# Kernel tuning notes

Measured on AMD Instinct MI355X. Metric: run time of the kernel, lower is better.

The kernel has to match this reference:

```python
import jax, jax.numpy as jnp
import numpy as np


def setup_inputs() -> dict:
    key = jax.random.key(0)
    k1, k2, k3, k4, k5 = jax.random.split(key, 5)
    B, C, Q, E = 16, 2048, 128, 200
    x_contexts = jax.random.normal(k1, (B, C, E), dtype=jnp.float32)
    x_questions = jax.random.normal(k2, (B, Q, E), dtype=jnp.float32)
    # nn.Linear(3E, 1, bias=False) weight: (1, 3E)
    w_sim = jax.random.normal(k3, (1, 3 * E), dtype=jnp.float32) * (1.0 / np.sqrt(3 * E))
    # nn.Linear(4E, 128) weight: (128, 4E), bias: (128,)
    w_proj = jax.random.normal(k4, (128, 4 * E), dtype=jnp.float32) * (1.0 / np.sqrt(4 * E))
    b_proj = jax.random.normal(k5, (128,), dtype=jnp.float32) * 0.01
    return {"x_contexts": x_contexts, "x_questions": x_questions,
            "w_sim": w_sim, "w_proj": w_proj, "b_proj": b_proj}


def reference(x_contexts, x_questions, w_sim, w_proj, b_proj):
    E = x_contexts.shape[-1]
    # Decompose w_sim . [c; q; c*q] into three small contractions — same math,
    # avoids materializing the (B, C, Q, 3E) broadcast tensor of the original.
    w1, w2, w3 = w_sim[0, :E], w_sim[0, E:2 * E], w_sim[0, 2 * E:]
    s_c = jnp.einsum('bce,e->bc', x_contexts, w1)            # (B, C)
    s_q = jnp.einsum('bqe,e->bq', x_questions, w2)           # (B, Q)
    s_cq = jnp.einsum('bce,bqe->bcq', x_contexts * w3, x_questions)  # (B, C, Q)
    scores = s_cq + s_c[:, :, None] + s_q[:, None, :]        # (B, C, Q)

    S1 = jax.nn.softmax(scores, axis=-1)   # softmax over question words
    S2 = jax.nn.softmax(scores, axis=-2)   # softmax over context words

    c2q = jnp.einsum('bcq,bqe->bce', S1, x_questions)        # (B, C, E)
    # q2c = (S1 @ S2^T) @ contexts; contract small E last to keep (B,C,C) single pass
    S1S2T = jnp.einsum('bcq,bdq->bcd', S1, S2)               # (B, C, C)
    q2c = jnp.einsum('bcd,bde->bce', S1S2T, x_contexts)      # (B, C, E)

    feats = jnp.concatenate(
        [x_contexts, c2q, x_contexts * c2q, x_contexts * q2c], axis=-1)  # (B, C, 4E)
    return jnp.einsum('bcf,of->bco', feats, w_proj) + b_proj  # (B, C, 128)
```

## Files before the change

kernel.cpp:

```cpp
#include <hip/hip_runtime.h>
#include <hip/hip_bf16.h>

#define Bn 16
#define Cn 2048
#define Qn 128
#define En 200
#define Fn 800
#define On 128
#define EP 208

typedef float f32x4 __attribute__((ext_vector_type(4)));
typedef __bf16 bf16x8 __attribute__((ext_vector_type(8)));

__device__ __forceinline__ unsigned short f2bf(float f) {
    union { float f; unsigned u; } v; v.f = f;
    unsigned r = v.u + 0x7FFF + ((v.u >> 16) & 1);
    return (unsigned short)(r >> 16);
}
__device__ __forceinline__ float bf2f(unsigned short h) {
    union { unsigned u; float f; } v; v.u = (unsigned)h << 16;
    return v.f;
}
__device__ __forceinline__ bf16x8 mul8(bf16x8 a, bf16x8 b) {
    bf16x8 o;
#pragma unroll
    for (int k = 0; k < 8; ++k) o[k] = (__bf16)((float)a[k] * (float)b[k]);
    return o;
}
__device__ __forceinline__ bf16x8 scale8(bf16x8 a, float s) {
    bf16x8 o;
#pragma unroll
    for (int k = 0; k < 8; ++k) o[k] = (__bf16)((float)a[k] * s);
    return o;
}

__global__ __launch_bounds__(256) void k_prep_all(const float* __restrict__ xq,
                                                  const float* __restrict__ wsim,
                                                  const float* __restrict__ wp,
                                                  const float* __restrict__ xc,
                                                  unsigned short* __restrict__ yqb,
                                                  float* __restrict__ s_q,
                                                  unsigned short* __restrict__ wpb,
                                                  unsigned short* __restrict__ xqaT,
                                                  unsigned short* __restrict__ xcb,
                                                  unsigned short* __restrict__ xcT) {
    int bx = blockIdx.x;
    if (bx < 512) {
        int wid = (bx * 256 + threadIdx.x) >> 6;
        int lane = threadIdx.x & 63;
        const float* xrow = xq + (size_t)wid * En;
        float s = 0.f;
        for (int e = lane; e < En; e += 64) {
            float x = xrow[e];
            yqb[(size_t)wid * En + e] = f2bf(x * wsim[400 + e] + wsim[e]);
            s += x * wsim[200 + e];
        }
        for (int i = 32; i; i >>= 1) s += __shfl_xor(s, i, 64);
        if (lane == 0) s_q[wid] = s;
    } else if (bx < 612) {
        int gid = (bx - 512) * 256 + threadIdx.x;
        int base = gid * 4;
        if (base < On * Fn) {
            float4 v = *(const float4*)(wp + base);
            ushort4 o;
            o.x = f2bf(v.x); o.y = f2bf(v.y); o.z = f2bf(v.z); o.w = f2bf(v.w);
            *(ushort4*)(wpb + base) = o;
        }
    } else if (bx < 740) {
        int lb = bx - 612;
        int et = lb & 3, qt = (lb >> 2) & 1, b = lb >> 3;
        int e0 = et * 64, q0 = qt * 64;
        int tid = threadIdx.x;
        __shared__ float t[64][65];
        for (int i = tid; i < 64 * 64; i += 256) {
            int qi = i >> 6, ei = i & 63;
            int e = e0 + ei;
            t[qi][ei] = (e < En) ? xq[((size_t)(b * Qn + q0 + qi)) * En + e] : 0.f;
        }
        __syncthreads();
        for (int i = tid; i < 64 * 64; i += 256) {
            int ei = i >> 6, qi = i & 63;
            int e = e0 + ei;
            if (e < En)
                xqaT[((size_t)(b * 400 + e)) * Qn + q0 + qi] = f2bf(t[qi][ei]);
        }
    } else {
        int lb = bx - 740;
        int ct = lb & 31, et = (lb >> 5) & 3, b = lb >> 7;
        int c0 = ct * 64, e0 = et * 64;
        int tid = threadIdx.x;
        __shared__ float t[64][65];
        for (int i = tid; i < 64 * 64; i += 256) {
            int ci = i >> 6, ei = i & 63;
            int e = e0 + ei;
            t[ci][ei] = (e < En) ? xc[((size_t)(b * Cn + c0 + ci)) * En + e] : 0.f;
        }
        __syncthreads();
        for (int i = tid; i < 64 * 16; i += 256) {
            int ci = i >> 4, g4 = (i & 15) * 4;
            int e = e0 + g4;
            if (e + 3 < En) {
                ushort4 o;
                o.x = f2bf(t[ci][g4]); o.y = f2bf(t[ci][g4 + 1]);
                o.z = f2bf(t[ci][g4 + 2]); o.w = f2bf(t[ci][g4 + 3]);
                *(ushort4*)(xcb + ((size_t)(b * Cn + c0 + ci)) * En + e) = o;
            }
        }
        for (int i = tid; i < 64 * 64; i += 256) {
            int ei = i >> 6, ci = i & 63;
            int e = e0 + ei;
            if (e < EP)
                xcT[((size_t)(b * EP + e)) * Cn + c0 + ci] = f2bf(t[ci][ei]);
        }
    }
}

__global__ __launch_bounds__(256) void k_scores_mfma(const unsigned short* __restrict__ xcb,
                                                     const unsigned short* __restrict__ yqb,
                                                     const float* __restrict__ s_q,
                                                     unsigned short* __restrict__ ET,
                                                     unsigned short* __restrict__ s1,
                                                     float* __restrict__ cpM,
                                                     float* __restrict__ cpS) {
    int b = blockIdx.y, blk = blockIdx.x, c0 = blk * 64;
    int w = threadIdx.x >> 6, lane = threadIdx.x & 63;
    int lrow = lane & 15, kg = lane >> 4;
    __shared__ float colm4[4][128];
    __shared__ float cols4[4][128];
    const unsigned short* Ab = xcb + ((size_t)(b * Cn + c0 + w * 16 + lrow)) * En + kg * 8;
    const unsigned short* Bb = yqb + ((size_t)(b * Qn + lrow)) * En + kg * 8;
    f32x4 acc[8] = {};
#pragma unroll
    for (int kc = 0; kc < 7; ++kc) {
        bool valid = (kc < 6) || (kg == 0);
        bf16x8 af = bf16x8{0,0,0,0,0,0,0,0};
        if (valid) af = *(const bf16x8*)(Ab + kc * 32);
        bf16x8 bfr[8];
#pragma unroll
        for (int j = 0; j < 8; ++j) {
            bfr[j] = bf16x8{0,0,0,0,0,0,0,0};
            if (valid) bfr[j] = *(const bf16x8*)(Bb + (size_t)j * 16 * En + kc * 32);
        }
#pragma unroll
        for (int j = 0; j < 8; ++j)
            acc[j] = __builtin_amdgcn_mfma_f32_16x16x32_bf16(af, bfr[j], acc[j], 0, 0, 0);
    }
#pragma unroll
    for (int j = 0; j < 8; ++j) {
        float sq = s_q[b * Qn + j * 16 + lrow];
#pragma unroll
        for (int r = 0; r < 4; ++r) acc[j][r] += sq;
    }
    float lm[8], ls[8];
#pragma unroll
    for (int j = 0; j < 8; ++j) {
        float m = fmaxf(fmaxf(acc[j][0], acc[j][1]), fmaxf(acc[j][2], acc[j][3]));
        m = fmaxf(m, __shfl_xor(m, 16, 64));
        m = fmaxf(m, __shfl_xor(m, 32, 64));
        lm[j] = m;
        float s = __expf(acc[j][0] - m) + __expf(acc[j][1] - m)
                + __expf(acc[j][2] - m) + __expf(acc[j][3] - m);
        s += __shfl_xor(s, 16, 64);
        s += __shfl_xor(s, 32, 64);
        ls[j] = s;
    }
    if (kg == 0) {
#pragma unroll
        for (int j = 0; j < 8; ++j) {
            colm4[w][j * 16 + lrow] = lm[j];
            cols4[w][j * 16 + lrow] = ls[j];
        }
    }
    __syncthreads();
    float mb[8];
#pragma unroll
    for (int j = 0; j < 8; ++j) {
        int q = j * 16 + lrow;
        float m = fmaxf(fmaxf(colm4[0][q], colm4[1][q]), fmaxf(colm4[2][q], colm4[3][q]));
        mb[j] = m;
        if (w == 0 && kg == 0) {
            float sb = cols4[0][q] * __expf(colm4[0][q] - m)
                     + cols4[1][q] * __expf(colm4[1][q] - m)
                     + cols4[2][q] * __expf(colm4[2][q] - m)
                     + cols4[3][q] * __expf(colm4[3][q] - m);
            cpM[(b * 32 + blk) * 128 + q] = m;
            cpS[(b * 32 + blk) * 128 + q] = sb;
        }
    }
#pragma unroll
    for (int j = 0; j < 8; ++j) {
        int q = j * 16 + lrow;
        ushort4 o;
        o.x = f2bf(__expf(acc[j][0] - mb[j]));
        o.y = f2bf(__expf(acc[j][1] - mb[j]));
        o.z = f2bf(__expf(acc[j][2] - mb[j]));
        o.w = f2bf(__expf(acc[j][3] - mb[j]));
        *(ushort4*)(ET + ((size_t)(b * Qn + q)) * Cn + c0 + w * 16 + kg * 4) = o;
    }
    size_t rowbase = (size_t)(b * Cn + c0 + w * 16 + kg * 4);
#pragma unroll
    for (int r = 0; r < 4; ++r) {
        float m = acc[0][r];
#pragma unroll
        for (int j = 1; j < 8; ++j) m = fmaxf(m, acc[j][r]);
        for (int d = 1; d < 16; d <<= 1) m = fmaxf(m, __shfl_xor(m, d, 64));
        float ssum = 0.f;
        float e[8];
#pragma unroll
        for (int j = 0; j < 8; ++j) {
            e[j] = __expf(acc[j][r] - m);
            ssum += e[j];
        }
        for (int d = 1; d < 16; d <<= 1) ssum += __shfl_xor(ssum, d, 64);
        float si = 1.f / ssum;
#pragma unroll
        for (int j = 0; j < 8; ++j)
            s1[(rowbase + r) * Qn + j * 16 + lrow] = f2bf(e[j] * si);
    }
}

__global__ __launch_bounds__(256) void k_a_part(const unsigned short* __restrict__ ET,
                                                const unsigned short* __restrict__ xcT,
                                                const float* __restrict__ cpM,
                                                const float* __restrict__ cpS,
                                                float* __restrict__ aP) {
    int mt = blockIdx.x, ks = blockIdx.y, b = blockIdx.z;
    int tid = threadIdx.x;
    int w = tid >> 6, lane = tid & 63;
    int lrow = lane & 15, kg = lane >> 4;
    __shared__ float colMs[128], colSis[128];
    if (tid < 128) {
        int q = tid;
        float m = -1e30f;
        for (int k = 0; k < 32; k++) m = fmaxf(m, cpM[(b * 32 + k) * 128 + q]);
        float s = 0.f;
        for (int k = 0; k < 32; k++) s += cpS[(b * 32 + k) * 128 + q] * __expf(cpM[(b * 32 + k) * 128 + q] - m);
        colMs[q] = m;
        colSis[q] = 1.f / s;
    }
    __syncthreads();
    int q0 = w * 16 + lrow, q1 = q0 + 64;
    int cb0 = ks * 8;
    float corr0[8], corr1[8];
#pragma unroll
    for (int i = 0; i < 8; ++i) {
        corr0[i] = __expf(cpM[(b * 32 + cb0 + i) * 128 + q0] - colMs[q0]) * colSis[q0];
        corr1[i] = __expf(cpM[(b * 32 + cb0 + i) * 128 + q1] - colMs[q1]) * colSis[q1];
    }
    const unsigned short* Ab = xcT + ((size_t)(b * EP + mt * 16 + lrow)) * Cn + ks * 512 + kg * 8;
    const unsigned short* B0 = ET + ((size_t)(b * Qn + q0)) * Cn + ks * 512 + kg * 8;
    const unsigned short* B1 = ET + ((size_t)(b * Qn + q1)) * Cn + ks * 512 + kg * 8;
    f32x4 acc0 = {}, acc1 = {};
#pragma unroll
    for (int kb = 0; kb < 4; ++kb) {
        bf16x8 af[4], bv0[4], bv1[4];
#pragma unroll
        for (int k4 = 0; k4 < 4; ++k4) {
            af[k4]  = *(const bf16x8*)(Ab + (kb * 4 + k4) * 32);
            bv0[k4] = *(const bf16x8*)(B0 + (kb * 4 + k4) * 32);
            bv1[k4] = *(const bf16x8*)(B1 + (kb * 4 + k4) * 32);
        }
#pragma unroll
        for (int k4 = 0; k4 < 4; ++k4) {
            bf16x8 s0 = scale8(bv0[k4], corr0[kb * 2 + (k4 >> 1)]);
            bf16x8 s1v = scale8(bv1[k4], corr1[kb * 2 + (k4 >> 1)]);
            acc0 = __builtin_amdgcn_mfma_f32_16x16x32_bf16(af[k4], s0, acc0, 0, 0, 0);
            acc1 = __builtin_amdgcn_mfma_f32_16x16x32_bf16(af[k4], s1v, acc1, 0, 0, 0);
        }
    }
    size_t ebase = (size_t)(b * 4 + ks) * EP + mt * 16 + kg * 4;
#pragma unroll
    for (int r = 0; r < 4; ++r) {
        aP[(ebase + r) * Qn + q0 - lrow + lrow] = acc0[r];
        aP[(ebase + r) * Qn + q1] = acc1[r];
    }
}

__global__ void k_acomb2(const float* __restrict__ aP, unsigned short* __restrict__ xqaT) {
    int gid = blockIdx.x * 256 + threadIdx.x;
    if (gid >= Bn * En * Qn) return;
    int b = gid / (En * Qn), r = gid % (En * Qn);
    int e = r / Qn, q = r % Qn;
    float s = 0.f;
#pragma unroll
    for (int k = 0; k < 4; k++)
        s += aP[((size_t)(b * 4 + k) * EP + e) * Qn + q];
    xqaT[((size_t)(b * 400 + 200 + e)) * Qn + q] = f2bf(s);
}

template<int NJ>
__device__ __forceinline__ void cq_phase64(const unsigned short* __restrict__ s1t,
                                           const unsigned short* __restrict__ xqaT_b,
                                           unsigned short* __restrict__ feats,
                                           int J0, int kg, int lrow) {
    f32x4 acc[NJ][4];
#pragma unroll
    for (int j = 0; j < NJ; ++j)
#pragma unroll
        for (int m = 0; m < 4; ++m) acc[j][m] = f32x4{0.f, 0.f, 0.f, 0.f};
#pragma unroll
    for (int kc = 0; kc < 4; ++kc) {
        bf16x8 a[4];
#pragma unroll
        for (int m = 0; m < 4; ++m)
            a[m] = *(const bf16x8*)(s1t + (m * 16 + lrow) * 136 + kg * 8 + kc * 32);
        bf16x8 bv[NJ];
#pragma unroll
        for (int j = 0; j < NJ; ++j)
            bv[j] = *(const bf16x8*)(xqaT_b + ((size_t)((J0 + j) * 16 + lrow)) * Qn + kg * 8 + kc * 32);
#pragma unroll
        for (int j = 0; j < NJ; ++j)
#pragma unroll
            for (int m = 0; m < 4; ++m)
                acc[j][m] = __builtin_amdgcn_mfma_f32_16x16x32_bf16(a[m], bv[j], acc[j][m], 0, 0, 0);
    }
#pragma unroll
    for (int j = 0; j < NJ; ++j) {
        int col = (J0 + j) * 16 + lrow;
        int off = col + (col < 200 ? 200 : 400);
#pragma unroll
        for (int m = 0; m < 4; ++m)
#pragma unroll
            for (int r = 0; r < 4; ++r)
                feats[(m * 16 + kg * 4 + r) * 808 + off] = f2bf(acc[j][m][r]);
    }
}

__global__ __launch_bounds__(512, 2) void k_tail(const unsigned short* __restrict__ s1,
                                                 const unsigned short* __restrict__ xqaT,
                                                 const unsigned short* __restrict__ xcb,
                                                 const unsigned short* __restrict__ wpb,
                                                 const float* __restrict__ bp,
                                                 float* __restrict__ out) {
    int b = blockIdx.y, c0 = blockIdx.x * 64;
    int tid = threadIdx.x;
    int w = tid >> 6, lane = tid & 63;
    int lrow = lane & 15, kg = lane >> 4;
    __shared__ unsigned short s1t[64 * 136];
    __shared__ unsigned short feats[64 * 808];

    for (int i = tid; i < 64 * 16; i += 512) {
        int row = i >> 4, c8 = i & 15;
        *(bf16x8*)(s1t + row * 136 + c8 * 8) =
            *(const bf16x8*)(s1 + ((size_t)(b * Cn + c0 + row)) * Qn + c8 * 8);
    }
    for (int i = tid; i < 64 * 25; i += 512) {
        int row = i / 25, e8 = (i % 25) * 8;
        *(bf16x8*)(feats + row * 808 + e8) =
            *(const bf16x8*)(xcb + ((size_t)(b * Cn + c0 + row)) * En + e8);
    }
    __syncthreads();

    {
        const unsigned short* xqaT_b = xqaT + (size_t)b * 400 * Qn;
        if (w < 7) cq_phase64<3>(s1t, xqaT_b, feats, w * 3, kg, lrow);
        else       cq_phase64<4>(s1t, xqaT_b, feats, 21, kg, lrow);
    }
    __syncthreads();

    for (int i = tid; i < 64 * 25; i += 512) {
        int row = i / 25, e8 = (i % 25) * 8;
        unsigned short* fr = feats + row * 808;
        bf16x8 x  = *(bf16x8*)(fr + e8);
        bf16x8 c2 = *(bf16x8*)(fr + 200 + e8);
        bf16x8 q2 = *(bf16x8*)(fr + 600 + e8);
        *(bf16x8*)(fr + 400 + e8) = mul8(x, c2);
        *(bf16x8*)(fr + 600 + e8) = mul8(x, q2);
    }
    __syncthreads();

    {
        f32x4 acc[4] = {};
        const unsigned short* Bb = wpb + ((size_t)(w * 16 + lrow)) * Fn + kg * 8;
        const unsigned short* A0 = feats + lrow * 808 + kg * 8;
#pragma unroll
        for (int kc = 0; kc < 25; ++kc) {
            bf16x8 bfr = *(const bf16x8*)(Bb + kc * 32);
#pragma unroll
            for (int m = 0; m < 4; ++m) {
                bf16x8 af = *(const bf16x8*)(A0 + m * 16 * 808 + kc * 32);
                acc[m] = __builtin_amdgcn_mfma_f32_16x16x32_bf16(af, bfr, acc[m], 0, 0, 0);
            }
        }
        int o = w * 16 + lrow;
        float bpv = bp[o];
#pragma unroll
        for (int m = 0; m < 4; ++m)
#pragma unroll
            for (int r = 0; r < 4; ++r)
                out[((size_t)(b * Cn + c0 + m * 16 + kg * 4 + r)) * On + o] = acc[m][r] + bpv;
    }
}

extern "C" void kernel_launch(void* const* d_in, const int* in_sizes, int n_in,
                              void* d_out, int out_size, void* d_ws, size_t ws_size,
                              hipStream_t stream) {
    const float* xc = (const float*)d_in[0];
    const float* xq = (const float*)d_in[1];
    const float* wsim = (const float*)d_in[2];
    const float* wp = (const float*)d_in[3];
    const float* bp = (const float*)d_in[4];
    float* out = (float*)d_out;
    float* ws = (float*)d_ws;

    unsigned short* ET_bf   = (unsigned short*)ws;
    unsigned short* s1_bf   = (unsigned short*)(ws + 2097152);
    unsigned short* xc_bf   = (unsigned short*)(ws + 4194304);
    unsigned short* xcT_bf  = (unsigned short*)(ws + 7471104);
    unsigned short* yq_bf   = (unsigned short*)(ws + 10878976);
    unsigned short* xqaT_bf = (unsigned short*)(ws + 11083776);
    unsigned short* wp_bf   = (unsigned short*)(ws + 11493376);
    float* s_q   = ws + 11544576;
    float* cpM   = ws + 11546624;
    float* cpS   = ws + 11612160;
    float* aP    = ws + 11677696;

    k_prep_all<<<2788, 256, 0, stream>>>(xq, wsim, wp, xc, yq_bf, s_q, wp_bf, xqaT_bf, xc_bf, xcT_bf);
    k_scores_mfma<<<dim3(32, 16), 256, 0, stream>>>(xc_bf, yq_bf, s_q, ET_bf, s1_bf, cpM, cpS);
    k_a_part<<<dim3(13, 4, 16), 256, 0, stream>>>(ET_bf, xcT_bf, cpM, cpS, aP);
    k_acomb2<<<1600, 256, 0, stream>>>(aP, xqaT_bf);
    k_tail<<<dim3(32, 16), 512, 0, stream>>>(s1_bf, xqaT_bf, xc_bf, wp_bf, bp, out);
}
```

Measured before the change: 95.80 us.

## Split tail projection into per-segment K-chunks to shrink shared memory

The tail kernel no longer builds a full 64x800 feature tile in shared memory. It keeps an x-context buffer and one reusable 64x224 buffer for c2q and then q2c, and accumulates the projection segment by segment. The x*c2q and x*q2c products are formed in registers right before each MFMA. The projection weights and the question-side matrices are repacked into zero-padded 224-wide segments so every K chunk is uniform, and launch bounds are raised to allow 4 blocks per CU. The aim is less LDS use and higher occupancy, at the cost of more barriers, some wasted MFMA work on the padding, and more register pressure under the tighter launch bound.

```diff
diff --git a/kernel.cpp b/kernel.cpp
--- a/kernel.cpp
+++ b/kernel.cpp
@@ -8,6 +8,9 @@
 #define Fn 800
 #define On 128
 #define EP 208
+#define KP 224
+#define XR 448
+#define CP 232
 
 typedef float f32x4 __attribute__((ext_vector_type(4)));
 typedef __bf16 bf16x8 __attribute__((ext_vector_type(8)));
@@ -40,7 +43,7 @@
                                                   const float* __restrict__ xc,
                                                   unsigned short* __restrict__ yqb,
                                                   float* __restrict__ s_q,
-                                                  unsigned short* __restrict__ wpb,
+                                                  unsigned short* __restrict__ wpP,
                                                   unsigned short* __restrict__ xqaT,
                                                   unsigned short* __restrict__ xcb,
                                                   unsigned short* __restrict__ xcT) {
@@ -57,17 +60,20 @@
         }
         for (int i = 32; i; i >>= 1) s += __shfl_xor(s, i, 64);
         if (lane == 0) s_q[wid] = s;
-    } else if (bx < 612) {
+    } else if (bx < 624) {
         int gid = (bx - 512) * 256 + threadIdx.x;
-        int base = gid * 4;
-        if (base < On * Fn) {
-            float4 v = *(const float4*)(wp + base);
-            ushort4 o;
-            o.x = f2bf(v.x); o.y = f2bf(v.y); o.z = f2bf(v.z); o.w = f2bf(v.w);
-            *(ushort4*)(wpb + base) = o;
-        }
-    } else if (bx < 740) {
-        int lb = bx - 612;
+        int flat = gid * 4;
+        int s = flat / (On * KP);
+        int rem = flat % (On * KP);
+        int o = rem / KP, k = rem % KP;
+        ushort4 ov = {0, 0, 0, 0};
+        if (k < 200) {
+            float4 v = *(const float4*)(wp + (size_t)o * Fn + s * 200 + k);
+            ov.x = f2bf(v.x); ov.y = f2bf(v.y); ov.z = f2bf(v.z); ov.w = f2bf(v.w);
+        }
+        *(ushort4*)(wpP + flat) = ov;
+    } else if (bx < 752) {
+        int lb = bx - 624;
         int et = lb & 3, qt = (lb >> 2) & 1, b = lb >> 3;
         int e0 = et * 64, q0 = qt * 64;
         int tid = threadIdx.x;
@@ -82,10 +88,20 @@
             int ei = i >> 6, qi = i & 63;
             int e = e0 + ei;
             if (e < En)
-                xqaT[((size_t)(b * 400 + e)) * Qn + q0 + qi] = f2bf(t[qi][ei]);
+                xqaT[((size_t)(b * XR + e)) * Qn + q0 + qi] = f2bf(t[qi][ei]);
+        }
+        if (et == 3) {
+            for (int i = tid; i < 24 * 64; i += 256) {
+                int e = 200 + (i >> 6), q = q0 + (i & 63);
+                xqaT[((size_t)(b * XR + e)) * Qn + q] = 0;
+            }
+            for (int i = tid; i < 24 * 64; i += 256) {
+                int e = 424 + (i >> 6), q = q0 + (i & 63);
+                xqaT[((size_t)(b * XR + e)) * Qn + q] = 0;
+            }
         }
     } else {
-        int lb = bx - 740;
+        int lb = bx - 752;
         int ct = lb & 31, et = (lb >> 5) & 3, b = lb >> 7;
         int c0 = ct * 64, e0 = et * 64;
         int tid = threadIdx.x;
@@ -271,7 +287,7 @@
     size_t ebase = (size_t)(b * 4 + ks) * EP + mt * 16 + kg * 4;
 #pragma unroll
     for (int r = 0; r < 4; ++r) {
-        aP[(ebase + r) * Qn + q0 - lrow + lrow] = acc0[r];
+        aP[(ebase + r) * Qn + q0] = acc0[r];
         aP[(ebase + r) * Qn + q1] = acc1[r];
     }
 }
@@ -285,14 +301,14 @@
 #pragma unroll
     for (int k = 0; k < 4; k++)
         s += aP[((size_t)(b * 4 + k) * EP + e) * Qn + q];
-    xqaT[((size_t)(b * 400 + 200 + e)) * Qn + q] = f2bf(s);
+    xqaT[((size_t)(b * XR + 224 + e)) * Qn + q] = f2bf(s);
 }
 
 template<int NJ>
-__device__ __forceinline__ void cq_phase64(const unsigned short* __restrict__ s1t,
-                                           const unsigned short* __restrict__ xqaT_b,
-                                           unsigned short* __restrict__ feats,
-                                           int J0, int kg, int lrow) {
+__device__ __forceinline__ void cq2(const unsigned short* __restrict__ s1t,
+                                    const unsigned short* __restrict__ xrows,
+                                    unsigned short* __restrict__ cbuf,
+                                    int J0, int kg, int lrow) {
     f32x4 acc[NJ][4];
 #pragma unroll
     for (int j = 0; j < NJ; ++j)
@@ -307,7 +323,7 @@
         bf16x8 bv[NJ];
 #pragma unroll
         for (int j = 0; j < NJ; ++j)
-            bv[j] = *(const bf16x8*)(xqaT_b + ((size_t)((J0 + j) * 16 + lrow)) * Qn + kg * 8 + kc * 32);
+            bv[j] = *(const bf16x8*)(xrows + ((size_t)((J0 + j) * 16 + lrow)) * Qn + kg * 8 + kc * 32);
 #pragma unroll
         for (int j = 0; j < NJ; ++j)
 #pragma unroll
@@ -317,19 +333,18 @@
 #pragma unroll
     for (int j = 0; j < NJ; ++j) {
         int col = (J0 + j) * 16 + lrow;
-        int off = col + (col < 200 ? 200 : 400);
 #pragma unroll
         for (int m = 0; m < 4; ++m)
 #pragma unroll
             for (int r = 0; r < 4; ++r)
-                feats[(m * 16 + kg * 4 + r) * 808 + off] = f2bf(acc[j][m][r]);
-    }
-}
-
-__global__ __launch_bounds__(512, 2) void k_tail(const unsigned short* __restrict__ s1,
+                cbuf[(m * 16 + kg * 4 + r) * CP + col] = f2bf(acc[j][m][r]);
+    }
+}
+
+__global__ __launch_bounds__(512, 4) void k_tail(const unsigned short* __restrict__ s1,
                                                  const unsigned short* __restrict__ xqaT,
                                                  const unsigned short* __restrict__ xcb,
-                                                 const unsigned short* __restrict__ wpb,
+                                                 const unsigned short* __restrict__ wpP,
                                                  const float* __restrict__ bp,
                                                  float* __restrict__ out) {
     int b = blockIdx.y, c0 = blockIdx.x * 64;
@@ -337,59 +352,92 @@
     int w = tid >> 6, lane = tid & 63;
     int lrow = lane & 15, kg = lane >> 4;
     __shared__ unsigned short s1t[64 * 136];
-    __shared__ unsigned short feats[64 * 808];
+    __shared__ unsigned short xbuf[64 * CP];
+    __shared__ unsigned short cbuf[64 * CP];
 
     for (int i = tid; i < 64 * 16; i += 512) {
         int row = i >> 4, c8 = i & 15;
         *(bf16x8*)(s1t + row * 136 + c8 * 8) =
             *(const bf16x8*)(s1 + ((size_t)(b * Cn + c0 + row)) * Qn + c8 * 8);
     }
-    for (int i = tid; i < 64 * 25; i += 512) {
-        int row = i / 25, e8 = (i % 25) * 8;
-        *(bf16x8*)(feats + row * 808 + e8) =
-            *(const bf16x8*)(xcb + ((size_t)(b * Cn + c0 + row)) * En + e8);
-    }
-    __syncthreads();
+    for (int i = tid; i < 64 * 28; i += 512) {
+        int row = i / 28, c8 = i % 28;
+        bf16x8 v = bf16x8{0,0,0,0,0,0,0,0};
+        if (c8 < 25) v = *(const bf16x8*)(xcb + ((size_t)(b * Cn + c0 + row)) * En + c8 * 8);
+        *(bf16x8*)(xbuf + row * CP + c8 * 8) = v;
+    }
+    __syncthreads();
+
+    f32x4 acc[4] = {};
+    const unsigned short* xq_b = xqaT + (size_t)b * XR * Qn;
+
+    if (w < 6)      cq2<2>(s1t, xq_b, cbuf, 2 * w, kg, lrow);
+    else if (w == 6) cq2<1>(s1t, xq_b, cbuf, 12, kg, lrow);
+    else             cq2<1>(s1t, xq_b, cbuf, 13, kg, lrow);
 
     {
-        const unsigned short* xqaT_b = xqaT + (size_t)b * 400 * Qn;
-        if (w < 7) cq_phase64<3>(s1t, xqaT_b, feats, w * 3, kg, lrow);
-        else       cq_phase64<4>(s1t, xqaT_b, feats, 21, kg, lrow);
-    }
-    __syncthreads();
-
-    for (int i = tid; i < 64 * 25; i += 512) {
-        int row = i / 25, e8 = (i % 25) * 8;
-        unsigned short* fr = feats + row * 808;
-        bf16x8 x  = *(bf16x8*)(fr + e8);
-        bf16x8 c2 = *(bf16x8*)(fr + 200 + e8);
-        bf16x8 q2 = *(bf16x8*)(fr + 600 + e8);
-        *(bf16x8*)(fr + 400 + e8) = mul8(x, c2);
-        *(bf16x8*)(fr + 600 + e8) = mul8(x, q2);
+        const unsigned short* B0 = wpP + ((size_t)(0 * On + w * 16 + lrow)) * KP + kg * 8;
+        const unsigned short* A0 = xbuf + lrow * CP + kg * 8;
+#pragma unroll
+        for (int kc = 0; kc < 7; ++kc) {
+            bf16x8 b0 = *(const bf16x8*)(B0 + kc * 32);
+#pragma unroll
+            for (int m = 0; m < 4; ++m) {
+                bf16x8 af = *(const bf16x8*)(A0 + m * 16 * CP + kc * 32);
+                acc[m] = __builtin_amdgcn_mfma_f32_16x16x32_bf16(af, b0, acc[m], 0, 0, 0);
+            }
+        }
     }
     __syncthreads();
 
     {
-        f32x4 acc[4] = {};
-        const unsigned short* Bb = wpb + ((size_t)(w * 16 + lrow)) * Fn + kg * 8;
-        const unsigned short* A0 = feats + lrow * 808 + kg * 8;
-#pragma unroll
-        for (int kc = 0; kc < 25; ++kc) {
-            bf16x8 bfr = *(const bf16x8*)(Bb + kc * 32);
+        const unsigned short* B1 = wpP + ((size_t)(1 * On + w * 16 + lrow)) * KP + kg * 8;
+        const unsigned short* B2 = wpP + ((size_t)(2 * On + w * 16 + lrow)) * KP + kg * 8;
+        const unsigned short* Ax = xbuf + lrow * CP + kg * 8;
+        const unsigned short* Ac = cbuf + lrow * CP + kg * 8;
+#pragma unroll
+        for (int kc = 0; kc < 7; ++kc) {
+            bf16x8 b1 = *(const bf16x8*)(B1 + kc * 32);
+            bf16x8 b2 = *(const bf16x8*)(B2 + kc * 32);
 #pragma unroll
             for (int m = 0; m < 4; ++m) {
-                bf16x8 af = *(const bf16x8*)(A0 + m * 16 * 808 + kc * 32);
-                acc[m] = __builtin_amdgcn_mfma_f32_16x16x32_bf16(af, bfr, acc[m], 0, 0, 0);
-            }
-        }
-        int o = w * 16 + lrow;
-        float bpv = bp[o];
-#pragma unroll
-        for (int m = 0; m < 4; ++m)
-#pragma unroll
-            for (int r = 0; r < 4; ++r)
-                out[((size_t)(b * Cn + c0 + m * 16 + kg * 4 + r)) * On + o] = acc[m][r] + bpv;
-    }
+                bf16x8 ac = *(const bf16x8*)(Ac + m * 16 * CP + kc * 32);
+                bf16x8 ax = *(const bf16x8*)(Ax + m * 16 * CP + kc * 32);
+                acc[m] = __builtin_amdgcn_mfma_f32_16x16x32_bf16(ac, b1, acc[m], 0, 0, 0);
+                acc[m] = __builtin_amdgcn_mfma_f32_16x16x32_bf16(mul8(ax, ac), b2, acc[m], 0, 0, 0);
+            }
+        }
+    }
+    __syncthreads();
+
+    if (w < 6)      cq2<2>(s1t, xq_b + (size_t)224 * Qn, cbuf, 2 * w, kg, lrow);
+    else if (w == 6) cq2<1>(s1t, xq_b + (size_t)224 * Qn, cbuf, 12, kg, lrow);
+    else             cq2<1>(s1t, xq_b + (size_t)224 * Qn, cbuf, 13, kg, lrow);
+    __syncthreads();
+
+    {
+        const unsigned short* B3 = wpP + ((size_t)(3 * On + w * 16 + lrow)) * KP + kg * 8;
+        const unsigned short* Ax = xbuf + lrow * CP + kg * 8;
+        const unsigned short* Ac = cbuf + lrow * CP + kg * 8;
+#pragma unroll
+        for (int kc = 0; kc < 7; ++kc) {
+            bf16x8 b3 = *(const bf16x8*)(B3 + kc * 32);
+#pragma unroll
+            for (int m = 0; m < 4; ++m) {
+                bf16x8 ac = *(const bf16x8*)(Ac + m * 16 * CP + kc * 32);
+                bf16x8 ax = *(const bf16x8*)(Ax + m * 16 * CP + kc * 32);
+                acc[m] = __builtin_amdgcn_mfma_f32_16x16x32_bf16(mul8(ax, ac), b3, acc[m], 0, 0, 0);
+            }
+        }
+    }
+
+    int o = w * 16 + lrow;
+    float bpv = bp[o];
+#pragma unroll
+    for (int m = 0; m < 4; ++m)
+#pragma unroll
+        for (int r = 0; r < 4; ++r)
+            out[((size_t)(b * Cn + c0 + m * 16 + kg * 4 + r)) * On + o] = acc[m][r] + bpv;
 }
 
 extern "C" void kernel_launch(void* const* d_in, const int* in_sizes, int n_in,
@@ -409,15 +457,15 @@
     unsigned short* xcT_bf  = (unsigned short*)(ws + 7471104);
     unsigned short* yq_bf   = (unsigned short*)(ws + 10878976);
     unsigned short* xqaT_bf = (unsigned short*)(ws + 11083776);
-    unsigned short* wp_bf   = (unsigned short*)(ws + 11493376);
-    float* s_q   = ws + 11544576;
-    float* cpM   = ws + 11546624;
-    float* cpS   = ws + 11612160;
-    float* aP    = ws + 11677696;
-
-    k_prep_all<<<2788, 256, 0, stream>>>(xq, wsim, wp, xc, yq_bf, s_q, wp_bf, xqaT_bf, xc_bf, xcT_bf);
+    unsigned short* wpP_bf  = (unsigned short*)(ws + 11542528);
+    float* s_q   = ws + 11599872;
+    float* cpM   = ws + 11601920;
+    float* cpS   = ws + 11667456;
+    float* aP    = ws + 11732992;
+
+    k_prep_all<<<2800, 256, 0, stream>>>(xq, wsim, wp, xc, yq_bf, s_q, wpP_bf, xqaT_bf, xc_bf, xcT_bf);
     k_scores_mfma<<<dim3(32, 16), 256, 0, stream>>>(xc_bf, yq_bf, s_q, ET_bf, s1_bf, cpM, cpS);
     k_a_part<<<dim3(13, 4, 16), 256, 0, stream>>>(ET_bf, xcT_bf, cpM, cpS, aP);
     k_acomb2<<<1600, 256, 0, stream>>>(aP, xqaT_bf);
-    k_tail<<<dim3(32, 16), 512, 0, stream>>>(s1_bf, xqaT_bf, xc_bf, wp_bf, bp, out);
-}
+    k_tail<<<dim3(32, 16), 512, 0, stream>>>(s1_bf, xqaT_bf, xc_bf, wpP_bf, bp, out);
+}
```

New measurement: 98.86 us. 1.03x slower.

## Fuse split-K partial GEMM and combine kernel via shared-memory reduction

Applied to the files above, without the earlier changes.

Reassigns the split-K dimension from grid blocks to the four waves within a block, and the grid y dimension now tiles the question axis. Partial results are reduced in shared memory and written directly as bf16 into xqaT, removing the k_acomb2 launch and the fp32 partial buffer round trip through global memory. In exchange, each block performs a shared-memory reduction plus an extra barrier, and each wave now computes a 16x16 question slice instead of the wider per-wave layout.

```diff
diff --git a/kernel.cpp b/kernel.cpp
--- a/kernel.cpp
+++ b/kernel.cpp
@@ -219,16 +219,17 @@
     }
 }
 
-__global__ __launch_bounds__(256) void k_a_part(const unsigned short* __restrict__ ET,
-                                                const unsigned short* __restrict__ xcT,
-                                                const float* __restrict__ cpM,
-                                                const float* __restrict__ cpS,
-                                                float* __restrict__ aP) {
-    int mt = blockIdx.x, ks = blockIdx.y, b = blockIdx.z;
+__global__ __launch_bounds__(256) void k_a_fused(const unsigned short* __restrict__ ET,
+                                                 const unsigned short* __restrict__ xcT,
+                                                 const float* __restrict__ cpM,
+                                                 const float* __restrict__ cpS,
+                                                 unsigned short* __restrict__ xqaT) {
+    int mt = blockIdx.x, qp = blockIdx.y, b = blockIdx.z;
     int tid = threadIdx.x;
     int w = tid >> 6, lane = tid & 63;
     int lrow = lane & 15, kg = lane >> 4;
     __shared__ float colMs[128], colSis[128];
+    __shared__ float red[4][2][16][16];
     if (tid < 128) {
         int q = tid;
         float m = -1e30f;
@@ -239,17 +240,17 @@
         colSis[q] = 1.f / s;
     }
     __syncthreads();
-    int q0 = w * 16 + lrow, q1 = q0 + 64;
-    int cb0 = ks * 8;
+    int q0 = qp * 16 + lrow, q1 = q0 + 64;
     float corr0[8], corr1[8];
 #pragma unroll
     for (int i = 0; i < 8; ++i) {
-        corr0[i] = __expf(cpM[(b * 32 + cb0 + i) * 128 + q0] - colMs[q0]) * colSis[q0];
-        corr1[i] = __expf(cpM[(b * 32 + cb0 + i) * 128 + q1] - colMs[q1]) * colSis[q1];
-    }
-    const unsigned short* Ab = xcT + ((size_t)(b * EP + mt * 16 + lrow)) * Cn + ks * 512 + kg * 8;
-    const unsigned short* B0 = ET + ((size_t)(b * Qn + q0)) * Cn + ks * 512 + kg * 8;
-    const unsigned short* B1 = ET + ((size_t)(b * Qn + q1)) * Cn + ks * 512 + kg * 8;
+        int cb = w * 8 + i;
+        corr0[i] = __expf(cpM[(b * 32 + cb) * 128 + q0] - colMs[q0]) * colSis[q0];
+        corr1[i] = __expf(cpM[(b * 32 + cb) * 128 + q1] - colMs[q1]) * colSis[q1];
+    }
+    const unsigned short* Ab = xcT + ((size_t)(b * EP + mt * 16 + lrow)) * Cn + w * 512 + kg * 8;
+    const unsigned short* B0 = ET + ((size_t)(b * Qn + q0)) * Cn + w * 512 + kg * 8;
+    const unsigned short* B1 = ET + ((size_t)(b * Qn + q1)) * Cn + w * 512 + kg * 8;
     f32x4 acc0 = {}, acc1 = {};
 #pragma unroll
     for (int kb = 0; kb < 4; ++kb) {
@@ -268,24 +269,24 @@
             acc1 = __builtin_amdgcn_mfma_f32_16x16x32_bf16(af[k4], s1v, acc1, 0, 0, 0);
         }
     }
-    size_t ebase = (size_t)(b * 4 + ks) * EP + mt * 16 + kg * 4;
 #pragma unroll
     for (int r = 0; r < 4; ++r) {
-        aP[(ebase + r) * Qn + q0 - lrow + lrow] = acc0[r];
-        aP[(ebase + r) * Qn + q1] = acc1[r];
-    }
-}
-
-__global__ void k_acomb2(const float* __restrict__ aP, unsigned short* __restrict__ xqaT) {
-    int gid = blockIdx.x * 256 + threadIdx.x;
-    if (gid >= Bn * En * Qn) return;
-    int b = gid / (En * Qn), r = gid % (En * Qn);
-    int e = r / Qn, q = r % Qn;
-    float s = 0.f;
-#pragma unroll
-    for (int k = 0; k < 4; k++)
-        s += aP[((size_t)(b * 4 + k) * EP + e) * Qn + q];
-    xqaT[((size_t)(b * 400 + 200 + e)) * Qn + q] = f2bf(s);
+        red[w][0][kg * 4 + r][lrow] = acc0[r];
+        red[w][1][kg * 4 + r][lrow] = acc1[r];
+    }
+    __syncthreads();
+#pragma unroll
+    for (int t = 0; t < 2; ++t) {
+        int idx = tid + t * 256;
+        int half = idx >> 8, rem = idx & 255;
+        int row = rem >> 4, col = rem & 15;
+        float s = red[0][half][row][col] + red[1][half][row][col]
+                + red[2][half][row][col] + red[3][half][row][col];
+        int e = mt * 16 + row;
+        int q = qp * 16 + half * 64 + col;
+        if (e < En)
+            xqaT[((size_t)(b * 400 + 200 + e)) * Qn + q] = f2bf(s);
+    }
 }
 
 template<int NJ>
@@ -413,11 +414,9 @@
     float* s_q   = ws + 11544576;
     float* cpM   = ws + 11546624;
     float* cpS   = ws + 11612160;
-    float* aP    = ws + 11677696;
 
     k_prep_all<<<2788, 256, 0, stream>>>(xq, wsim, wp, xc, yq_bf, s_q, wp_bf, xqaT_bf, xc_bf, xcT_bf);
     k_scores_mfma<<<dim3(32, 16), 256, 0, stream>>>(xc_bf, yq_bf, s_q, ET_bf, s1_bf, cpM, cpS);
-    k_a_part<<<dim3(13, 4, 16), 256, 0, stream>>>(ET_bf, xcT_bf, cpM, cpS, aP);
-    k_acomb2<<<1600, 256, 0, stream>>>(aP, xqaT_bf);
+    k_a_fused<<<dim3(13, 4, 16), 256, 0, stream>>>(ET_bf, xcT_bf, cpM, cpS, xqaT_bf);
     k_tail<<<dim3(32, 16), 512, 0, stream>>>(s1_bf, xqaT_bf, xc_bf, wp_bf, bp, out);
 }
```

Result: no change. 94.51 us (-1.3%).
